# Kernel optimization log

Measured on AMD Instinct MI355X. Metric: run time of the kernel, lower is better.

## Reference

```python
import jax, jax.numpy as jnp
import numpy as np

NQ, NK = 32, 128          # block height / width (AF3 local attention)
INF = 1.0e9
EPS = 1e-5


def _ln(x, w=None, b=None):
    m = jnp.mean(x, axis=-1, keepdims=True)
    v = jnp.var(x, axis=-1, keepdims=True)
    y = (x - m) * jax.lax.rsqrt(v + EPS)
    if w is not None:
        y = y * w
    if b is not None:
        y = y + b
    return y


def _key_idx(N):
    # For query block i, keys cover a window of NK atoms centered on the block.
    nb = N // NQ
    start = np.arange(nb)[:, None] * NQ - (NK - NQ) // 2
    idx = start + np.arange(NK)[None, :]          # [nb, NK]
    valid = ((idx >= 0) & (idx < N)).astype(np.float32)
    return np.clip(idx, 0, N - 1), valid


def setup_inputs() -> dict:
    key = jax.random.key(0)
    ks = iter(jax.random.split(key, 32))
    B, N, C, CZ, H, CH, CS = 4, 8192, 128, 16, 4, 32, 128
    nb = N // NQ
    nrm = lambda sh, sc=0.02: jax.random.normal(next(ks), sh, jnp.float32) * sc
    return dict(
        a=nrm((B, N, C), 1.0),
        z=nrm((B, nb, NQ, NK, CZ), 1.0),
        s=nrm((B, N, CS), 1.0),
        mask=jnp.ones((B, N), jnp.float32),
        ln_s_q_w=jnp.ones((CS,), jnp.float32),
        Wg_q=nrm((CS, C)), bg_q=jnp.zeros((C,), jnp.float32), Wb_q=nrm((CS, C)),
        ln_s_k_w=jnp.ones((CS,), jnp.float32),
        Wg_k=nrm((CS, C)), bg_k=jnp.zeros((C,), jnp.float32), Wb_k=nrm((CS, C)),
        ln_z_w=jnp.ones((CZ,), jnp.float32), ln_z_b=jnp.zeros((CZ,), jnp.float32),
        W_z=nrm((CZ, H)),
        Wq=nrm((C, H * CH)), Wk=nrm((C, H * CH)), Wv=nrm((C, H * CH)),
        Wg=nrm((C, H * CH)), bg=jnp.ones((H * CH,), jnp.float32),
        Wo=nrm((H * CH, C)), bo=jnp.zeros((C,), jnp.float32),
        W_ado=nrm((CS, C)), b_ado=jnp.full((C,), -2.0, jnp.float32),
    )


def reference(a, z, s, mask,
              ln_s_q_w, Wg_q, bg_q, Wb_q,
              ln_s_k_w, Wg_k, bg_k, Wb_k,
              ln_z_w, ln_z_b, W_z,
              Wq, Wk, Wv, Wg, bg, Wo, bo,
              W_ado, b_ado):
    B, N, C = a.shape
    H = W_z.shape[1]
    CH = Wq.shape[1] // H
    nb = N // NQ
    idx, valid = _key_idx(N)

    # --- block inputs ---
    a_q = a.reshape(B, nb, NQ, C)            # [B, nb, NQ, C]
    a_k = a[:, idx]                          # [B, nb, NK, C]
    q_mask = mask.reshape(B, nb, NQ)
    k_mask = mask[:, idx] * valid            # [B, nb, NK]
    pair_mask = q_mask[..., :, None] * k_mask[..., None, :]   # [B, nb, NQ, NK]
    mask_bias = (INF * (pair_mask - 1.0))[..., None, :, :]     # [B, nb, 1, NQ, NK]

    # --- pair bias from z ---
    zb = _ln(z, ln_z_w, ln_z_b) @ W_z        # [B, nb, NQ, NK, H]
    zb = jnp.moveaxis(zb, -1, -3)            # [B, nb, H, NQ, NK]

    # --- AdaLN conditioning ---
    s_q = s.reshape(B, nb, NQ, -1)
    s_k = s[:, idx]
    sqn = _ln(s_q, ln_s_q_w)
    skn = _ln(s_k, ln_s_k_w)
    aq = jax.nn.sigmoid(sqn @ Wg_q + bg_q) * _ln(a_q) + sqn @ Wb_q
    ak = jax.nn.sigmoid(skn @ Wg_k + bg_k) * _ln(a_k) + skn @ Wb_k

    # --- blocked attention with pair bias ---
    scale = 1.0 / np.sqrt(CH).astype(np.float32)
    q = (aq @ Wq).reshape(B, nb, NQ, H, CH) * scale
    k = (ak @ Wk).reshape(B, nb, NK, H, CH)
    v = (ak @ Wv).reshape(B, nb, NK, H, CH)
    logits = jnp.einsum('bnqhc,bnkhc->bnhqk', q, k) + mask_bias + zb
    attn = jax.nn.softmax(logits, axis=-1)
    o = jnp.einsum('bnhqk,bnkhc->bnqhc', attn, v)
    g = jax.nn.sigmoid(aq @ Wg + bg).reshape(B, nb, NQ, H, CH)
    o = (g * o).reshape(B, nb, NQ, H * CH)
    out = (o @ Wo + bo).reshape(B, N, C)[:, :N, :]

    # --- AdaLN-Zero output gate ---
    out = jax.nn.sigmoid(s @ W_ado + b_ado) * out
    return out
```

## Files before the change

kernel.cpp:

```cpp
#include <hip/hip_runtime.h>
#include <cstdint>
#include <cstddef>

#define B_ 4
#define N_ 8192
#define C_ 128
#define NB_ 256
#define EPS_ 1e-5f

typedef unsigned int u32;
typedef unsigned short u16;

typedef short bf16x8 __attribute__((ext_vector_type(8)));
typedef float f32x4 __attribute__((ext_vector_type(4)));
union U16x8 { uint4 u4; bf16x8 v; };

__device__ __forceinline__ float bf2f(u16 v){ union{u32 i; float f;} x; x.i = ((u32)v)<<16; return x.f; }
__device__ __forceinline__ u16 f2bf(float f){ union{float f; u32 i;} x; x.f=f; u32 r = x.i + 0x7fffu + ((x.i>>16)&1u); return (u16)(r>>16); }
__device__ __forceinline__ u32 pk2(float a, float b){ return (u32)f2bf(a) | ((u32)f2bf(b)<<16); }
__device__ __forceinline__ float sigm(float x){ return 1.f/(1.f+__expf(-x)); }

__global__ void k0_prep(const float* __restrict__ Wgq, const float* __restrict__ Wbq,
                        const float* __restrict__ Wgk, const float* __restrict__ Wbk,
                        const float* __restrict__ Wado, const float* __restrict__ Wq_,
                        const float* __restrict__ Wg_, const float* __restrict__ Wk_,
                        const float* __restrict__ Wv_, const float* __restrict__ Wo_,
                        const float* __restrict__ lnsqw, const float* __restrict__ lnskw,
                        u16* __restrict__ PW, float* __restrict__ AUX)
{
  if (blockIdx.x < 80) {
    int gid = blockIdx.x*256 + threadIdx.x;
    int mat = gid >> 11;
    int rem = gid & 2047;
    int ks = rem >> 9;
    int rem2 = rem & 511;
    int nt = rem2 >> 6;
    int lane = rem2 & 63;
    int kbase = ks*32 + (lane>>4)*8;
    int n = nt*16 + (lane&15);
    const float* W; int scmode = 0; float fixed = 1.f;
    switch (mat) {
      case 0: W = Wgq; scmode = 1; break;
      case 1: W = Wbq; scmode = 1; break;
      case 2: W = Wgk; scmode = 2; break;
      case 3: W = Wbk; scmode = 2; break;
      case 4: W = Wado; break;
      case 5: W = Wq_; fixed = 0.17677669529663687f; break;
      case 6: W = Wg_; break;
      case 7: W = Wk_; break;
      case 8: W = Wv_; break;
      default: W = Wo_; break;
    }
    u16 o[8];
    #pragma unroll
    for (int j=0;j<8;j++){
      int k = kbase + j;
      float sc = fixed;
      if (scmode == 1) sc *= lnsqw[k];
      else if (scmode == 2) sc *= lnskw[k];
      o[j] = f2bf(W[k*128 + n] * sc);
    }
    uint4 pk;
    pk.x = (u32)o[0] | ((u32)o[1]<<16); pk.y = (u32)o[2] | ((u32)o[3]<<16);
    pk.z = (u32)o[4] | ((u32)o[5]<<16); pk.w = (u32)o[6] | ((u32)o[7]<<16);
    *(uint4*)(PW + (size_t)gid*8) = pk;
  } else {
    int t = threadIdx.x;
    if (t < 128) {
      float s = 0.f;
      for (int k=0;k<128;k++) s += Wado[k*128 + t];
      AUX[t] = s;
    }
  }
}

__device__ __forceinline__ void mm_single(f32x4 acc[4][2], const u16* Abase, const u16* __restrict__ PW,
                                          int mat, int wave, int lane, int lq, int quad)
{
  #pragma unroll
  for (int ks=0; ks<4; ks++){
    U16x8 b0, b1;
    b0.u4 = *(const uint4*)(PW + (size_t)((((mat*4+ks)*8) + wave*2+0)*64 + lane)*8);
    b1.u4 = *(const uint4*)(PW + (size_t)((((mat*4+ks)*8) + wave*2+1)*64 + lane)*8);
    #pragma unroll
    for (int mt=0; mt<4; mt++){
      U16x8 a; a.u4 = *(const uint4*)(Abase + (mt*16+lq)*136 + ks*32 + quad*8);
      acc[mt][0] = __builtin_amdgcn_mfma_f32_16x16x32_bf16(a.v, b0.v, acc[mt][0], 0,0,0);
      acc[mt][1] = __builtin_amdgcn_mfma_f32_16x16x32_bf16(a.v, b1.v, acc[mt][1], 0,0,0);
    }
  }
}
__device__ __forceinline__ void mm_dual(f32x4 acc1[4][2], int m1, f32x4 acc2[4][2], int m2,
                                        const u16* Abase, const u16* __restrict__ PW,
                                        int wave, int lane, int lq, int quad)
{
  #pragma unroll
  for (int ks=0; ks<4; ks++){
    U16x8 b10, b11, b20, b21;
    b10.u4 = *(const uint4*)(PW + (size_t)((((m1*4+ks)*8) + wave*2+0)*64 + lane)*8);
    b11.u4 = *(const uint4*)(PW + (size_t)((((m1*4+ks)*8) + wave*2+1)*64 + lane)*8);
    b20.u4 = *(const uint4*)(PW + (size_t)((((m2*4+ks)*8) + wave*2+0)*64 + lane)*8);
    b21.u4 = *(const uint4*)(PW + (size_t)((((m2*4+ks)*8) + wave*2+1)*64 + lane)*8);
    #pragma unroll
    for (int mt=0; mt<4; mt++){
      U16x8 a; a.u4 = *(const uint4*)(Abase + (mt*16+lq)*136 + ks*32 + quad*8);
      acc1[mt][0] = __builtin_amdgcn_mfma_f32_16x16x32_bf16(a.v, b10.v, acc1[mt][0], 0,0,0);
      acc1[mt][1] = __builtin_amdgcn_mfma_f32_16x16x32_bf16(a.v, b11.v, acc1[mt][1], 0,0,0);
      acc2[mt][0] = __builtin_amdgcn_mfma_f32_16x16x32_bf16(a.v, b20.v, acc2[mt][0], 0,0,0);
      acc2[mt][1] = __builtin_amdgcn_mfma_f32_16x16x32_bf16(a.v, b21.v, acc2[mt][1], 0,0,0);
    }
  }
}
#define ZERO82(A) do{ _Pragma("unroll") for(int _m=0;_m<4;_m++){ A[_m][0]=(f32x4)(0.f); A[_m][1]=(f32x4)(0.f);} }while(0)

__global__ __launch_bounds__(256, 2)
void kf_fused(const float* __restrict__ ga, const float* __restrict__ gs,
              const float* __restrict__ gz, const float* __restrict__ gmask,
              const float* __restrict__ lnzw, const float* __restrict__ lnzb,
              const float* __restrict__ Wz,
              const float* __restrict__ bgq, const float* __restrict__ bgk,
              const float* __restrict__ bg, const float* __restrict__ bado,
              const u16* __restrict__ PW, const float* __restrict__ AUX,
              u16* __restrict__ Q, u16* __restrict__ K, u16* __restrict__ VT,
              u16* __restrict__ G, u16* __restrict__ ADO, u16* __restrict__ ZB)
{
  __shared__ char arena[52736];
  const int blk = (int)blockIdx.x;
  const int mod = blk % 3;
  const int tid = (int)threadIdx.x;

  if (mod != 2) {
    u16* ZT   = (u16*)arena;
    float* WZL = (float*)(arena + 36864);
    float* QMV = (float*)(arena + 37152);
    float* KMV = (float*)(arena + 37280);
    const int bi = (blk/3)*2 + mod;
    const int b = bi >> 8, i = bi & 255;

    if (tid < 64) WZL[tid] = lnzw[tid>>2] * Wz[tid];
    else if (tid < 68) { int h = tid-64; float s=0.f; for (int c=0;c<16;c++) s += lnzw[c]*Wz[c*4+h]; WZL[64+h]=s; }
    else if (tid < 72) { int h = tid-68; float s=0.f; for (int c=0;c<16;c++) s += lnzb[c]*Wz[c*4+h]; WZL[68+h]=s; }
    else if (tid >= 96 && tid < 128) QMV[tid-96] = gmask[(size_t)b*N_ + i*32 + (tid-96)];
    else if (tid >= 128) {
      int k = tid - 128;
      int raw = i*32 - 48 + k;
      KMV[k] = (raw >= 0 && raw < N_) ? gmask[(size_t)b*N_ + raw] : 0.f;
    }
    __syncthreads();

    #pragma unroll 1
    for (int it=0; it<16; ++it){
      int g = it*256 + tid;
      const float* zp = gz + (size_t)bi*65536 + (size_t)g*16;
      float4 z0 = *(const float4*)(zp);
      float4 z1 = *(const float4*)(zp+4);
      float4 z2 = *(const float4*)(zp+8);
      float4 z3 = *(const float4*)(zp+12);
      int q = g >> 7, key = g & 127;
      float zv[16] = {z0.x,z0.y,z0.z,z0.w, z1.x,z1.y,z1.z,z1.w,
                      z2.x,z2.y,z2.z,z2.w, z3.x,z3.y,z3.z,z3.w};
      float sm=0.f, sq=0.f, S0=0.f, S1=0.f, S2=0.f, S3=0.f;
      #pragma unroll
      for (int c=0;c<16;c++){
        sm += zv[c]; sq = fmaf(zv[c],zv[c],sq);
        S0 = fmaf(zv[c], WZL[c*4+0], S0); S1 = fmaf(zv[c], WZL[c*4+1], S1);
        S2 = fmaf(zv[c], WZL[c*4+2], S2); S3 = fmaf(zv[c], WZL[c*4+3], S3);
      }
      float mz = sm*(1.f/16.f);
      float rz = rsqrtf(sq*(1.f/16.f) - mz*mz + EPS_);
      float mb = 1000000000.0f*(QMV[q]*KMV[key] - 1.f);
      int base = key*36 + q;
      ZT[0*4608 + base] = f2bf((S0 - mz*WZL[64])*rz + WZL[68] + mb);
      ZT[1*4608 + base] = f2bf((S1 - mz*WZL[65])*rz + WZL[69] + mb);
      ZT[2*4608 + base] = f2bf((S2 - mz*WZL[66])*rz + WZL[70] + mb);
      ZT[3*4608 + base] = f2bf((S3 - mz*WZL[67])*rz + WZL[71] + mb);
    }
    __syncthreads();

    u16* dst = ZB + (size_t)bi*16384;
    const int key = tid >> 1, q0 = (tid & 1)*16;
    #pragma unroll
    for (int h=0; h<4; h++){
      const u16* src = ZT + h*4608 + key*36 + q0;
      uint2 w0 = *(const uint2*)(src);
      uint2 w1 = *(const uint2*)(src+4);
      uint2 w2 = *(const uint2*)(src+8);
      uint2 w3 = *(const uint2*)(src+12);
      uint4 o0; o0.x=w0.x; o0.y=w0.y; o0.z=w1.x; o0.w=w1.y;
      uint4 o1; o1.x=w2.x; o1.y=w2.y; o1.z=w3.x; o1.w=w3.y;
      *(uint4*)(dst + h*4096 + tid*16)     = o0;
      *(uint4*)(dst + h*4096 + tid*16 + 8) = o1;
    }
    return;
  }

  u16* SN  = (u16*)arena;
  u16* LNA = (u16*)(arena + 17408);
  u16* AQ  = (u16*)(arena + 34816);
  float* SSTAT = (float*)(arena + 52224);

  const int rowbase = (blk/3) * 64;
  const int b = rowbase >> 13;
  const int nb0 = rowbase & 8191;
  const int wave = tid >> 6, lane = tid & 63;
  const int lq = lane & 15, quad = lane >> 4;

  {
    const float* sbase = gs + (size_t)rowbase*128;
    const float* abase = ga + (size_t)rowbase*128;
    #pragma unroll 1
    for (int t=0;t<8;t++){
      int chunk = t*256 + tid;
      int row = chunk >> 5;
      int k4 = (chunk & 31) * 4;
      float4 vs = *(const float4*)(sbase + (size_t)chunk*4);
      float4 va = *(const float4*)(abase + (size_t)chunk*4);
      float sm = vs.x+vs.y+vs.z+vs.w, sq = vs.x*vs.x+vs.y*vs.y+vs.z*vs.z+vs.w*vs.w;
      float am = va.x+va.y+va.z+va.w, a2 = va.x*va.x+va.y*va.y+va.z*va.z+va.w*va.w;
      #pragma unroll
      for (int m=1;m<32;m<<=1){
        sm += __shfl_xor(sm,m,32); sq += __shfl_xor(sq,m,32);
        am += __shfl_xor(am,m,32); a2 += __shfl_xor(a2,m,32);
      }
      float smean = sm*(1.f/128.f);
      float svar  = sq*(1.f/128.f) - smean*smean;
      float srstd = rsqrtf(svar + EPS_);
      float amean = am*(1.f/128.f);
      float avar  = a2*(1.f/128.f) - amean*amean;
      float arstd = rsqrtf(avar + EPS_);
      *(uint2*)(SN + row*136 + k4) = make_uint2(
        pk2((vs.x-smean)*srstd,(vs.y-smean)*srstd), pk2((vs.z-smean)*srstd,(vs.w-smean)*srstd));
      *(uint2*)(LNA + row*136 + k4) = make_uint2(
        pk2((va.x-amean)*arstd,(va.y-amean)*arstd), pk2((va.z-amean)*arstd,(va.w-amean)*arstd));
      if ((tid & 31) == 0){
        SSTAT[row*2]   = smean;
        SSTAT[row*2+1] = (svar + EPS_)*srstd;
      }
    }
  }
  __syncthreads();

  const int cg0 = wave*32 + lq;
  const int cg1 = cg0 + 16;

  {
    f32x4 acc[4][2]; ZERO82(acc);
    mm_single(acc, SN, PW, 4, wave, lane, lq, quad);
    float cs0 = AUX[cg0], cs1 = AUX[cg1];
    float bb0 = bado[cg0], bb1 = bado[cg1];
    #pragma unroll
    for (int mt=0; mt<4; mt++){
      #pragma unroll
      for (int reg=0; reg<4; reg++){
        int row = mt*16 + quad*4 + reg;
        float mean = SSTAT[row*2], std = SSTAT[row*2+1];
        ADO[(size_t)(rowbase+row)*128 + cg0] = f2bf(sigm(std*acc[mt][0][reg] + mean*cs0 + bb0));
        ADO[(size_t)(rowbase+row)*128 + cg1] = f2bf(sigm(std*acc[mt][1][reg] + mean*cs1 + bb1));
      }
    }
  }

  {
    f32x4 aG[4][2], aB[4][2]; ZERO82(aG); ZERO82(aB);
    mm_dual(aG, 0, aB, 1, SN, PW, wave, lane, lq, quad);
    float bq0 = bgq[cg0], bq1 = bgq[cg1];
    #pragma unroll
    for (int mt=0; mt<4; mt++){
      #pragma unroll
      for (int reg=0; reg<4; reg++){
        int row = mt*16 + quad*4 + reg;
        float l0 = bf2f(LNA[row*136 + cg0]), l1 = bf2f(LNA[row*136 + cg1]);
        AQ[row*136 + cg0] = f2bf(sigm(aG[mt][0][reg]+bq0)*l0 + aB[mt][0][reg]);
        AQ[row*136 + cg1] = f2bf(sigm(aG[mt][1][reg]+bq1)*l1 + aB[mt][1][reg]);
      }
    }
  }

  {
    f32x4 aG[4][2], aB[4][2]; ZERO82(aG); ZERO82(aB);
    mm_dual(aG, 2, aB, 3, SN, PW, wave, lane, lq, quad);
    float bk0 = bgk[cg0], bk1 = bgk[cg1];
    #pragma unroll
    for (int mt=0; mt<4; mt++){
      #pragma unroll
      for (int reg=0; reg<4; reg++){
        int row = mt*16 + quad*4 + reg;
        float l0 = bf2f(LNA[row*136 + cg0]), l1 = bf2f(LNA[row*136 + cg1]);
        aG[mt][0][reg] = sigm(aG[mt][0][reg]+bk0)*l0 + aB[mt][0][reg];
        aG[mt][1][reg] = sigm(aG[mt][1][reg]+bk1)*l1 + aB[mt][1][reg];
      }
    }
    __syncthreads();
    #pragma unroll
    for (int mt=0; mt<4; mt++){
      #pragma unroll
      for (int reg=0; reg<4; reg++){
        int row = mt*16 + quad*4 + reg;
        SN[row*136 + cg0] = f2bf(aG[mt][0][reg]);
        SN[row*136 + cg1] = f2bf(aG[mt][1][reg]);
      }
    }
    __syncthreads();
  }

  {
    f32x4 aQ_[4][2], aG_[4][2]; ZERO82(aQ_); ZERO82(aG_);
    mm_dual(aQ_, 5, aG_, 6, AQ, PW, wave, lane, lq, quad);
    float bg0 = bg[cg0], bg1 = bg[cg1];
    #pragma unroll
    for (int mt=0; mt<4; mt++){
      #pragma unroll
      for (int reg=0; reg<4; reg++){
        int row = mt*16 + quad*4 + reg;
        Q[(size_t)(rowbase+row)*128 + cg0] = f2bf(aQ_[mt][0][reg]);
        Q[(size_t)(rowbase+row)*128 + cg1] = f2bf(aQ_[mt][1][reg]);
        G[(size_t)(rowbase+row)*128 + cg0] = f2bf(sigm(aG_[mt][0][reg]+bg0));
        G[(size_t)(rowbase+row)*128 + cg1] = f2bf(sigm(aG_[mt][1][reg]+bg1));
      }
    }
  }

  {
    f32x4 aK_[4][2], aV_[4][2]; ZERO82(aK_); ZERO82(aV_);
    mm_dual(aK_, 7, aV_, 8, SN, PW, wave, lane, lq, quad);
    #pragma unroll
    for (int mt=0; mt<4; mt++){
      #pragma unroll
      for (int reg=0; reg<4; reg++){
        int row = mt*16 + quad*4 + reg;
        K[(size_t)(rowbase+row)*128 + cg0] = f2bf(aK_[mt][0][reg]);
        K[(size_t)(rowbase+row)*128 + cg1] = f2bf(aK_[mt][1][reg]);
      }
      ushort4 p0, p1;
      p0.x = f2bf(aV_[mt][0][0]); p0.y = f2bf(aV_[mt][0][1]);
      p0.z = f2bf(aV_[mt][0][2]); p0.w = f2bf(aV_[mt][0][3]);
      p1.x = f2bf(aV_[mt][1][0]); p1.y = f2bf(aV_[mt][1][1]);
      p1.z = f2bf(aV_[mt][1][2]); p1.w = f2bf(aV_[mt][1][3]);
      int nloc = nb0 + mt*16 + quad*4;
      *(ushort4*)(VT + ((size_t)(b*128 + cg0))*N_ + nloc) = p0;
      *(ushort4*)(VT + ((size_t)(b*128 + cg1))*N_ + nloc) = p1;
    }
  }
}

__global__ __launch_bounds__(256, 4)
void k2_attn(const float* __restrict__ bo,
             const u16* __restrict__ PW,
             const u16* __restrict__ Q, const u16* __restrict__ K,
             const u16* __restrict__ VT, const u16* __restrict__ G,
             const u16* __restrict__ ADO, const u16* __restrict__ ZB,
             float* __restrict__ gout)
{
  __shared__ char arena[34816];
  u16* ATTall = (u16*)arena;
  u16* GO     = (u16*)arena;

  const int flat = (int)blockIdx.x;
  const int x = flat & 7, r = flat >> 3;
  const int j = r & 31, b = r >> 5;
  const int i = x*32 + j;

  const int tid = (int)threadIdx.x;
  const int wave = tid >> 6, lane = tid & 63;
  const int lq = lane & 15, quad = lane >> 4;
  const int h = wave;
  const int start = i*32 - 48;
  u16* ATT = ATTall + h*(32*136);

  f32x4 L[2][8];
  #pragma unroll
  for (int mt=0;mt<2;mt++) for (int nt=0;nt<8;nt++) L[mt][nt] = (f32x4)(0.f);
  {
    U16x8 aQ[2];
    #pragma unroll
    for (int mt=0;mt<2;mt++)
      aQ[mt].u4 = *(const uint4*)(Q + ((size_t)b*N_ + i*32 + mt*16 + lq)*128 + h*32 + quad*8);
    #pragma unroll
    for (int nt=0;nt<8;nt++){
      int kr = min(max(start + nt*16 + lq, 0), N_-1);
      U16x8 bk; bk.u4 = *(const uint4*)(K + ((size_t)b*N_ + kr)*128 + h*32 + quad*8);
      L[0][nt] = __builtin_amdgcn_mfma_f32_16x16x32_bf16(aQ[0].v, bk.v, L[0][nt], 0,0,0);
      L[1][nt] = __builtin_amdgcn_mfma_f32_16x16x32_bf16(aQ[1].v, bk.v, L[1][nt], 0,0,0);
    }
  }

  {
    const u16* zbb = ZB + (size_t)(b*NB_ + i)*16384 + h*4096;
    #pragma unroll
    for (int nt=0;nt<8;nt++){
      #pragma unroll
      for (int mt=0;mt<2;mt++){
        ushort4 z4 = *(const ushort4*)(zbb + (nt*16+lq)*32 + mt*16 + quad*4);
        L[mt][nt][0] += bf2f(z4.x); L[mt][nt][1] += bf2f(z4.y);
        L[mt][nt][2] += bf2f(z4.z); L[mt][nt][3] += bf2f(z4.w);
      }
    }
  }

  #pragma unroll
  for (int mt=0;mt<2;mt++){
    #pragma unroll
    for (int reg=0;reg<4;reg++){
      float mx = -3.0e38f;
      #pragma unroll
      for (int nt=0;nt<8;nt++) mx = fmaxf(mx, L[mt][nt][reg]);
      mx = fmaxf(mx, __shfl_xor(mx,1,16));
      mx = fmaxf(mx, __shfl_xor(mx,2,16));
      mx = fmaxf(mx, __shfl_xor(mx,4,16));
      mx = fmaxf(mx, __shfl_xor(mx,8,16));
      float e[8]; float s = 0.f;
      #pragma unroll
      for (int nt=0;nt<8;nt++){ e[nt] = __expf(L[mt][nt][reg]-mx); s += e[nt]; }
      s += __shfl_xor(s,1,16);
      s += __shfl_xor(s,2,16);
      s += __shfl_xor(s,4,16);
      s += __shfl_xor(s,8,16);
      float inv = 1.f/s;
      int q = mt*16 + quad*4 + reg;
      #pragma unroll
      for (int nt=0;nt<8;nt++) ATT[q*136 + nt*16 + lq] = f2bf(e[nt]*inv);
    }
  }

  f32x4 O[2][2];
  O[0][0]=(f32x4)(0.f); O[0][1]=(f32x4)(0.f); O[1][0]=(f32x4)(0.f); O[1][1]=(f32x4)(0.f);
  #pragma unroll
  for (int ks=0;ks<4;ks++){
    U16x8 ba[2];
    #pragma unroll
    for (int nt=0;nt<2;nt++)
      ba[nt].u4 = *(const uint4*)(ATT + (nt*16+lq)*136 + ks*32 + quad*8);
    int kk = start + ks*32 + quad*8;
    kk = min(max(kk,0), N_-8);
    #pragma unroll
    for (int mt=0;mt<2;mt++){
      U16x8 av;
      av.u4 = *(const uint4*)(VT + ((size_t)(b*128 + h*32 + mt*16 + lq))*N_ + kk);
      O[mt][0] = __builtin_amdgcn_mfma_f32_16x16x32_bf16(av.v, ba[0].v, O[mt][0], 0,0,0);
      O[mt][1] = __builtin_amdgcn_mfma_f32_16x16x32_bf16(av.v, ba[1].v, O[mt][1], 0,0,0);
    }
  }
  __syncthreads();

  #pragma unroll
  for (int mt=0;mt<2;mt++){
    #pragma unroll
    for (int nt=0;nt<2;nt++){
      int q = nt*16 + lq;
      int cb = h*32 + mt*16 + quad*4;
      ushort4 g4 = *(const ushort4*)(G + ((size_t)b*N_ + i*32 + q)*128 + cb);
      ushort4 p;
      p.x = f2bf(bf2f(g4.x)*O[mt][nt][0]); p.y = f2bf(bf2f(g4.y)*O[mt][nt][1]);
      p.z = f2bf(bf2f(g4.z)*O[mt][nt][2]); p.w = f2bf(bf2f(g4.w)*O[mt][nt][3]);
      *(ushort4*)(GO + q*136 + cb) = p;
    }
  }
  __syncthreads();

  {
    f32x4 U[2][2];
    U[0][0]=(f32x4)(0.f); U[0][1]=(f32x4)(0.f); U[1][0]=(f32x4)(0.f); U[1][1]=(f32x4)(0.f);
    #pragma unroll
    for (int ks=0;ks<4;ks++){
      U16x8 b0, b1;
      b0.u4 = *(const uint4*)(PW + (size_t)((((9*4+ks)*8) + wave*2+0)*64 + lane)*8);
      b1.u4 = *(const uint4*)(PW + (size_t)((((9*4+ks)*8) + wave*2+1)*64 + lane)*8);
      #pragma unroll
      for (int mt=0;mt<2;mt++){
        U16x8 a; a.u4 = *(const uint4*)(GO + (mt*16+lq)*136 + ks*32 + quad*8);
        U[mt][0] = __builtin_amdgcn_mfma_f32_16x16x32_bf16(a.v, b0.v, U[mt][0], 0,0,0);
        U[mt][1] = __builtin_amdgcn_mfma_f32_16x16x32_bf16(a.v, b1.v, U[mt][1], 0,0,0);
      }
    }
    const int cg0 = wave*32 + lq, cg1 = cg0 + 16;
    float b00 = bo[cg0], b01 = bo[cg1];
    #pragma unroll
    for (int mt=0;mt<2;mt++){
      #pragma unroll
      for (int reg=0;reg<4;reg++){
        int q = mt*16 + quad*4 + reg;
        size_t rowoff = ((size_t)b*N_ + i*32 + q)*128;
        float ad0 = bf2f(ADO[rowoff + cg0]);
        float ad1 = bf2f(ADO[rowoff + cg1]);
        gout[rowoff + cg0] = ad0*(U[mt][0][reg] + b00);
        gout[rowoff + cg1] = ad1*(U[mt][1][reg] + b01);
      }
    }
  }
}

extern "C" void kernel_launch(void* const* d_in, const int* in_sizes, int n_in,
                              void* d_out, int out_size, void* d_ws, size_t ws_size,
                              hipStream_t stream) {
  (void)in_sizes; (void)n_in; (void)out_size; (void)ws_size;
  const float* ga    = (const float*)d_in[0];
  const float* gz    = (const float*)d_in[1];
  const float* gs    = (const float*)d_in[2];
  const float* gmask = (const float*)d_in[3];
  const float* lnsqw = (const float*)d_in[4];
  const float* Wgq   = (const float*)d_in[5];
  const float* bgq   = (const float*)d_in[6];
  const float* Wbq   = (const float*)d_in[7];
  const float* lnskw = (const float*)d_in[8];
  const float* Wgk   = (const float*)d_in[9];
  const float* bgk   = (const float*)d_in[10];
  const float* Wbk   = (const float*)d_in[11];
  const float* lnzw  = (const float*)d_in[12];
  const float* lnzb  = (const float*)d_in[13];
  const float* Wz    = (const float*)d_in[14];
  const float* Wq    = (const float*)d_in[15];
  const float* Wk    = (const float*)d_in[16];
  const float* Wv    = (const float*)d_in[17];
  const float* Wg    = (const float*)d_in[18];
  const float* bg    = (const float*)d_in[19];
  const float* Wo    = (const float*)d_in[20];
  const float* bo    = (const float*)d_in[21];
  const float* Wado  = (const float*)d_in[22];
  const float* bado  = (const float*)d_in[23];

  char* ws = (char*)d_ws;
  u16* Qb  = (u16*)(ws + 0);
  u16* Kb  = (u16*)(ws + 8388608);
  u16* VTb = (u16*)(ws + 16777216);
  u16* Gb  = (u16*)(ws + 25165824);
  u16* ADOb= (u16*)(ws + 33554432);
  u16* ZBb = (u16*)(ws + 41943040);
  u16* PW  = (u16*)(ws + 75497472);
  float* AUX = (float*)(ws + 75497472 + 327680);

  k0_prep<<<81, 256, 0, stream>>>(Wgq, Wbq, Wgk, Wbk, Wado, Wq, Wg, Wk, Wv, Wo,
                                  lnsqw, lnskw, PW, AUX);
  kf_fused<<<1536, 256, 0, stream>>>(ga, gs, gz, gmask, lnzw, lnzb, Wz,
                                     bgq, bgk, bg, bado, PW, AUX,
                                     Qb, Kb, VTb, Gb, ADOb, ZBb);
  k2_attn<<<1024, 256, 0, stream>>>(bo, PW, Qb, Kb, VTb, Gb, ADOb, ZBb, (float*)d_out);
}
```

Baseline: 470.2 us.

## Fuse pair-bias computation into attention kernel, removing ZB round trip

Moves the z layer-norm and pair-bias projection out of the combined projection kernel and into the attention kernel, computing the bias tile in shared memory right before the logits. This drops the bf16 ZB intermediate write and re-read through global memory and simplifies the projection launch to 512 blocks. In exchange the attention kernel carries the large z read and extra LDS use and syncs, which may reduce occupancy and lose the previous overlap of z work with the projections.

```diff
diff --git a/kernel.cpp b/kernel.cpp
--- a/kernel.cpp
+++ b/kernel.cpp
@@ -114,92 +114,21 @@
 #define ZERO82(A) do{ _Pragma("unroll") for(int _m=0;_m<4;_m++){ A[_m][0]=(f32x4)(0.f); A[_m][1]=(f32x4)(0.f);} }while(0)
 
 __global__ __launch_bounds__(256, 2)
-void kf_fused(const float* __restrict__ ga, const float* __restrict__ gs,
-              const float* __restrict__ gz, const float* __restrict__ gmask,
-              const float* __restrict__ lnzw, const float* __restrict__ lnzb,
-              const float* __restrict__ Wz,
-              const float* __restrict__ bgq, const float* __restrict__ bgk,
-              const float* __restrict__ bg, const float* __restrict__ bado,
-              const u16* __restrict__ PW, const float* __restrict__ AUX,
-              u16* __restrict__ Q, u16* __restrict__ K, u16* __restrict__ VT,
-              u16* __restrict__ G, u16* __restrict__ ADO, u16* __restrict__ ZB)
+void k1_proj(const float* __restrict__ ga, const float* __restrict__ gs,
+             const float* __restrict__ bgq, const float* __restrict__ bgk,
+             const float* __restrict__ bg, const float* __restrict__ bado,
+             const u16* __restrict__ PW, const float* __restrict__ AUX,
+             u16* __restrict__ Q, u16* __restrict__ K, u16* __restrict__ VT,
+             u16* __restrict__ G, u16* __restrict__ ADO)
 {
   __shared__ char arena[52736];
-  const int blk = (int)blockIdx.x;
-  const int mod = blk % 3;
-  const int tid = (int)threadIdx.x;
-
-  if (mod != 2) {
-    u16* ZT   = (u16*)arena;
-    float* WZL = (float*)(arena + 36864);
-    float* QMV = (float*)(arena + 37152);
-    float* KMV = (float*)(arena + 37280);
-    const int bi = (blk/3)*2 + mod;
-    const int b = bi >> 8, i = bi & 255;
-
-    if (tid < 64) WZL[tid] = lnzw[tid>>2] * Wz[tid];
-    else if (tid < 68) { int h = tid-64; float s=0.f; for (int c=0;c<16;c++) s += lnzw[c]*Wz[c*4+h]; WZL[64+h]=s; }
-    else if (tid < 72) { int h = tid-68; float s=0.f; for (int c=0;c<16;c++) s += lnzb[c]*Wz[c*4+h]; WZL[68+h]=s; }
-    else if (tid >= 96 && tid < 128) QMV[tid-96] = gmask[(size_t)b*N_ + i*32 + (tid-96)];
-    else if (tid >= 128) {
-      int k = tid - 128;
-      int raw = i*32 - 48 + k;
-      KMV[k] = (raw >= 0 && raw < N_) ? gmask[(size_t)b*N_ + raw] : 0.f;
-    }
-    __syncthreads();
-
-    #pragma unroll 1
-    for (int it=0; it<16; ++it){
-      int g = it*256 + tid;
-      const float* zp = gz + (size_t)bi*65536 + (size_t)g*16;
-      float4 z0 = *(const float4*)(zp);
-      float4 z1 = *(const float4*)(zp+4);
-      float4 z2 = *(const float4*)(zp+8);
-      float4 z3 = *(const float4*)(zp+12);
-      int q = g >> 7, key = g & 127;
-      float zv[16] = {z0.x,z0.y,z0.z,z0.w, z1.x,z1.y,z1.z,z1.w,
-                      z2.x,z2.y,z2.z,z2.w, z3.x,z3.y,z3.z,z3.w};
-      float sm=0.f, sq=0.f, S0=0.f, S1=0.f, S2=0.f, S3=0.f;
-      #pragma unroll
-      for (int c=0;c<16;c++){
-        sm += zv[c]; sq = fmaf(zv[c],zv[c],sq);
-        S0 = fmaf(zv[c], WZL[c*4+0], S0); S1 = fmaf(zv[c], WZL[c*4+1], S1);
-        S2 = fmaf(zv[c], WZL[c*4+2], S2); S3 = fmaf(zv[c], WZL[c*4+3], S3);
-      }
-      float mz = sm*(1.f/16.f);
-      float rz = rsqrtf(sq*(1.f/16.f) - mz*mz + EPS_);
-      float mb = 1000000000.0f*(QMV[q]*KMV[key] - 1.f);
-      int base = key*36 + q;
-      ZT[0*4608 + base] = f2bf((S0 - mz*WZL[64])*rz + WZL[68] + mb);
-      ZT[1*4608 + base] = f2bf((S1 - mz*WZL[65])*rz + WZL[69] + mb);
-      ZT[2*4608 + base] = f2bf((S2 - mz*WZL[66])*rz + WZL[70] + mb);
-      ZT[3*4608 + base] = f2bf((S3 - mz*WZL[67])*rz + WZL[71] + mb);
-    }
-    __syncthreads();
-
-    u16* dst = ZB + (size_t)bi*16384;
-    const int key = tid >> 1, q0 = (tid & 1)*16;
-    #pragma unroll
-    for (int h=0; h<4; h++){
-      const u16* src = ZT + h*4608 + key*36 + q0;
-      uint2 w0 = *(const uint2*)(src);
-      uint2 w1 = *(const uint2*)(src+4);
-      uint2 w2 = *(const uint2*)(src+8);
-      uint2 w3 = *(const uint2*)(src+12);
-      uint4 o0; o0.x=w0.x; o0.y=w0.y; o0.z=w1.x; o0.w=w1.y;
-      uint4 o1; o1.x=w2.x; o1.y=w2.y; o1.z=w3.x; o1.w=w3.y;
-      *(uint4*)(dst + h*4096 + tid*16)     = o0;
-      *(uint4*)(dst + h*4096 + tid*16 + 8) = o1;
-    }
-    return;
-  }
-
   u16* SN  = (u16*)arena;
   u16* LNA = (u16*)(arena + 17408);
   u16* AQ  = (u16*)(arena + 34816);
   float* SSTAT = (float*)(arena + 52224);
 
-  const int rowbase = (blk/3) * 64;
+  const int tid = (int)threadIdx.x;
+  const int rowbase = (int)blockIdx.x * 64;
   const int b = rowbase >> 13;
   const int nb0 = rowbase & 8191;
   const int wave = tid >> 6, lane = tid & 63;
@@ -344,21 +273,27 @@
 }
 
 __global__ __launch_bounds__(256, 4)
-void k2_attn(const float* __restrict__ bo,
+void k2_attn(const float* __restrict__ gz, const float* __restrict__ gmask,
+             const float* __restrict__ lnzw, const float* __restrict__ lnzb,
+             const float* __restrict__ Wz, const float* __restrict__ bo,
              const u16* __restrict__ PW,
              const u16* __restrict__ Q, const u16* __restrict__ K,
              const u16* __restrict__ VT, const u16* __restrict__ G,
-             const u16* __restrict__ ADO, const u16* __restrict__ ZB,
-             float* __restrict__ gout)
+             const u16* __restrict__ ADO, float* __restrict__ gout)
 {
-  __shared__ char arena[34816];
+  __shared__ char arena[37888];
+  u16* ZT     = (u16*)arena;
   u16* ATTall = (u16*)arena;
   u16* GO     = (u16*)arena;
+  float* WZL  = (float*)(arena + 36864);
+  float* QMV  = (float*)(arena + 37152);
+  float* KMV  = (float*)(arena + 37280);
 
   const int flat = (int)blockIdx.x;
   const int x = flat & 7, r = flat >> 3;
   const int j = r & 31, b = r >> 5;
   const int i = x*32 + j;
+  const int bi = b*NB_ + i;
 
   const int tid = (int)threadIdx.x;
   const int wave = tid >> 6, lane = tid & 63;
@@ -367,6 +302,46 @@
   const int start = i*32 - 48;
   u16* ATT = ATTall + h*(32*136);
 
+  if (tid < 64) WZL[tid] = lnzw[tid>>2] * Wz[tid];
+  else if (tid < 68) { int hh = tid-64; float s=0.f; for (int c=0;c<16;c++) s += lnzw[c]*Wz[c*4+hh]; WZL[64+hh]=s; }
+  else if (tid < 72) { int hh = tid-68; float s=0.f; for (int c=0;c<16;c++) s += lnzb[c]*Wz[c*4+hh]; WZL[68+hh]=s; }
+  else if (tid >= 96 && tid < 128) QMV[tid-96] = gmask[(size_t)b*N_ + i*32 + (tid-96)];
+  else if (tid >= 128) {
+    int k = tid - 128;
+    int raw = start + k;
+    KMV[k] = (raw >= 0 && raw < N_) ? gmask[(size_t)b*N_ + raw] : 0.f;
+  }
+  __syncthreads();
+
+  #pragma unroll 2
+  for (int it=0; it<16; ++it){
+    int g = it*256 + tid;
+    const float* zp = gz + (size_t)bi*65536 + (size_t)g*16;
+    float4 z0 = *(const float4*)(zp);
+    float4 z1 = *(const float4*)(zp+4);
+    float4 z2 = *(const float4*)(zp+8);
+    float4 z3 = *(const float4*)(zp+12);
+    int q = g >> 7, key = g & 127;
+    float zv[16] = {z0.x,z0.y,z0.z,z0.w, z1.x,z1.y,z1.z,z1.w,
+                    z2.x,z2.y,z2.z,z2.w, z3.x,z3.y,z3.z,z3.w};
+    float sm=0.f, sq=0.f, S0=0.f, S1=0.f, S2=0.f, S3=0.f;
+    #pragma unroll
+    for (int c=0;c<16;c++){
+      sm += zv[c]; sq = fmaf(zv[c],zv[c],sq);
+      S0 = fmaf(zv[c], WZL[c*4+0], S0); S1 = fmaf(zv[c], WZL[c*4+1], S1);
+      S2 = fmaf(zv[c], WZL[c*4+2], S2); S3 = fmaf(zv[c], WZL[c*4+3], S3);
+    }
+    float mz = sm*(1.f/16.f);
+    float rz = rsqrtf(sq*(1.f/16.f) - mz*mz + EPS_);
+    float mb = 1000000000.0f*(QMV[q]*KMV[key] - 1.f);
+    int base = key*36 + q;
+    ZT[0*4608 + base] = f2bf((S0 - mz*WZL[64])*rz + WZL[68] + mb);
+    ZT[1*4608 + base] = f2bf((S1 - mz*WZL[65])*rz + WZL[69] + mb);
+    ZT[2*4608 + base] = f2bf((S2 - mz*WZL[66])*rz + WZL[70] + mb);
+    ZT[3*4608 + base] = f2bf((S3 - mz*WZL[67])*rz + WZL[71] + mb);
+  }
+  __syncthreads();
+
   f32x4 L[2][8];
   #pragma unroll
   for (int mt=0;mt<2;mt++) for (int nt=0;nt<8;nt++) L[mt][nt] = (f32x4)(0.f);
@@ -384,18 +359,16 @@
     }
   }
 
-  {
-    const u16* zbb = ZB + (size_t)(b*NB_ + i)*16384 + h*4096;
-    #pragma unroll
-    for (int nt=0;nt<8;nt++){
-      #pragma unroll
-      for (int mt=0;mt<2;mt++){
-        ushort4 z4 = *(const ushort4*)(zbb + (nt*16+lq)*32 + mt*16 + quad*4);
-        L[mt][nt][0] += bf2f(z4.x); L[mt][nt][1] += bf2f(z4.y);
-        L[mt][nt][2] += bf2f(z4.z); L[mt][nt][3] += bf2f(z4.w);
-      }
-    }
-  }
+  #pragma unroll
+  for (int nt=0;nt<8;nt++){
+    #pragma unroll
+    for (int mt=0;mt<2;mt++){
+      ushort4 z4 = *(const ushort4*)(ZT + h*4608 + (nt*16+lq)*36 + mt*16 + quad*4);
+      L[mt][nt][0] += bf2f(z4.x); L[mt][nt][1] += bf2f(z4.y);
+      L[mt][nt][2] += bf2f(z4.z); L[mt][nt][3] += bf2f(z4.w);
+    }
+  }
+  __syncthreads();
 
   #pragma unroll
   for (int mt=0;mt<2;mt++){
@@ -524,14 +497,13 @@
   u16* VTb = (u16*)(ws + 16777216);
   u16* Gb  = (u16*)(ws + 25165824);
   u16* ADOb= (u16*)(ws + 33554432);
-  u16* ZBb = (u16*)(ws + 41943040);
-  u16* PW  = (u16*)(ws + 75497472);
-  float* AUX = (float*)(ws + 75497472 + 327680);
+  u16* PW  = (u16*)(ws + 41943040);
+  float* AUX = (float*)(ws + 41943040 + 327680);
 
   k0_prep<<<81, 256, 0, stream>>>(Wgq, Wbq, Wgk, Wbk, Wado, Wq, Wg, Wk, Wv, Wo,
                                   lnsqw, lnskw, PW, AUX);
-  kf_fused<<<1536, 256, 0, stream>>>(ga, gs, gz, gmask, lnzw, lnzb, Wz,
-                                     bgq, bgk, bg, bado, PW, AUX,
-                                     Qb, Kb, VTb, Gb, ADOb, ZBb);
-  k2_attn<<<1024, 256, 0, stream>>>(bo, PW, Qb, Kb, VTb, Gb, ADOb, ZBb, (float*)d_out);
+  k1_proj<<<512, 256, 0, stream>>>(ga, gs, bgq, bgk, bg, bado, PW, AUX,
+                                   Qb, Kb, VTb, Gb, ADOb);
+  k2_attn<<<1024, 256, 0, stream>>>(gz, gmask, lnzw, lnzb, Wz, bo, PW,
+                                    Qb, Kb, VTb, Gb, ADOb, (float*)d_out);
 }
```

Measured after the change: 462.2 us. No clear change (-1.7%).
